# Optimization experiments

Measured on AMD Instinct MI355X. Metric: run time of the kernel, lower is better.

Reference implementation:

```python
import jax, jax.numpy as jnp
import numpy as np


def _pointnet(x, w1, b1, w2, b2, w3, b3):
    # x: [B, 3, P]; shared per-point MLP 3->64->128->128, max-pool over points -> [B,128]
    h = jax.nn.relu(jnp.einsum('oc,bcp->bop', w1, x) + b1[None, :, None])
    h = jax.nn.relu(jnp.einsum('oc,bcp->bop', w2, h) + b2[None, :, None])
    h = jax.nn.relu(jnp.einsum('oc,bcp->bop', w3, h) + b3[None, :, None])
    return h.max(axis=2)


def _lstm_layer(x, wih, whh, b):
    # x: [B, T, D]; standard LSTM (pytorch gate order i,f,g,o), returns [B, T, 128]
    B = x.shape[0]
    h0 = jnp.zeros((B, 128), x.dtype)
    def step(carry, xt):
        h, c = carry
        g = xt @ wih.T + h @ whh.T + b
        i, f, gg, o = jnp.split(g, 4, axis=-1)
        c = jax.nn.sigmoid(f) * c + jax.nn.sigmoid(i) * jnp.tanh(gg)
        h = jax.nn.sigmoid(o) * jnp.tanh(c)
        return (h, c), h
    _, hs = jax.lax.scan(step, (h0, h0), jnp.swapaxes(x, 0, 1))
    return jnp.swapaxes(hs, 0, 1)


def _edgeconv(x, aff, tw, tb, pw, pb, N):
    # DGL EdgeConv, max aggregation. Edges: det i -> track (N+j) where aff[i,j]==1, plus
    # self loops on every node. Message on edge u->v: theta(x_u - x_v) + phi(x_v).
    phi = x @ pw.T + pb                                   # [N+M, 256]
    diff = x[:N][:, None, :] - x[N:][None, :, :]          # [N, M, 256] (x_src - x_dst)
    msg = jnp.einsum('nmc,oc->nmo', diff, tw) + tb        # theta applied to diffs
    msg = jnp.where(aff[:, :, None] > 0, msg, jnp.finfo(x.dtype).min)
    h_trk = phi[N:] + jnp.maximum(tb, msg.max(axis=0))    # self-loop message is theta(0)=tb
    h_det = phi[:N] + tb                                  # dets only receive their self loop
    return jnp.concatenate([h_det, h_trk], axis=0)


def _forward(det_pc_in_box, det_boxes3d, track_pc_in_box, track_boxes3d, init_aff_matrix,
             pn_w1, pn_b1, pn_w2, pn_b2, pn_w3, pn_b3,
             mlp_w1, mlp_b1, mlp_w2, mlp_b2,
             l0_wih, l0_whh, l0_b, l1_wih, l1_whh, l1_b,
             ec_tw, ec_tb, ec_pw, ec_pb,
             er_w1, er_b1, er_w2, er_b2):
    N = det_pc_in_box.shape[0]
    det_app = _pointnet(jnp.swapaxes(det_pc_in_box, 1, 2), pn_w1, pn_b1, pn_w2, pn_b2, pn_w3, pn_b3)
    trk_app = _pointnet(jnp.swapaxes(track_pc_in_box, 1, 2), pn_w1, pn_b1, pn_w2, pn_b2, pn_w3, pn_b3)
    det_mot = jax.nn.relu(det_boxes3d @ mlp_w1.T + mlp_b1) @ mlp_w2.T + mlp_b2
    trk_mot = _lstm_layer(_lstm_layer(track_boxes3d, l0_wih, l0_whh, l0_b), l1_wih, l1_whh, l1_b)[:, -1, :]
    h = jnp.concatenate([jnp.concatenate([det_app, det_mot], axis=1),
                         jnp.concatenate([trk_app, trk_mot], axis=1)], axis=0)  # [N+M, 256]
    for k in range(4):
        h = jax.nn.relu(_edgeconv(h, init_aff_matrix, ec_tw[k], ec_tb[k], ec_pw[k], ec_pb[k], N))
    # pairwise affinity: (track - det) differences through small MLP + sigmoid (BCE head)
    edges = h[N:][None, :, :] - h[:N][:, None, :]                                # [N, M, 256]
    e = jax.nn.relu(jnp.einsum('nmc,oc->nmo', edges, er_w1) + er_b1)             # [N, M, 64]
    regr = jax.nn.sigmoid(jnp.einsum('nmo,ko->nmk', e, er_w2) + er_b2)[..., 0]   # [N, M]
    valid = init_aff_matrix * regr
    valid = jnp.where(valid == 0, jnp.asarray(99.0, valid.dtype), valid)
    return valid


def setup_inputs() -> dict:
    key = jax.random.key(0)
    ks = jax.random.split(key, 20)
    N, M, P, T = 512, 512, 256, 10
    f = jnp.float32
    def rn(k, shp):
        return jax.random.normal(k, shp, dtype=f) * 0.05
    return {
        'det_pc_in_box': jax.random.normal(ks[0], (N, P, 3), dtype=f),
        'det_boxes3d': jax.random.normal(ks[1], (N, 9), dtype=f),
        'track_pc_in_box': jax.random.normal(ks[2], (M, P, 3), dtype=f),
        'track_boxes3d': jax.random.normal(ks[3], (M, T, 9), dtype=f),
        'init_aff_matrix': jnp.ones((N, M), dtype=f),
        'gt_affinity_matrix': jnp.zeros((N, M), dtype=jnp.int32),
        'pn_w1': rn(ks[4], (64, 3)), 'pn_b1': jnp.zeros((64,), f),
        'pn_w2': rn(ks[5], (128, 64)), 'pn_b2': jnp.zeros((128,), f),
        'pn_w3': rn(ks[6], (128, 128)), 'pn_b3': jnp.zeros((128,), f),
        'mlp_w1': rn(ks[7], (64, 9)), 'mlp_b1': jnp.zeros((64,), f),
        'mlp_w2': rn(ks[8], (128, 64)), 'mlp_b2': jnp.zeros((128,), f),
        'l0_wih': rn(ks[9], (512, 9)), 'l0_whh': rn(ks[10], (512, 128)), 'l0_b': jnp.zeros((512,), f),
        'l1_wih': rn(ks[11], (512, 128)), 'l1_whh': rn(ks[12], (512, 128)), 'l1_b': jnp.zeros((512,), f),
        'ec_tw': rn(ks[13], (4, 256, 256)), 'ec_tb': jnp.zeros((4, 256), f),
        'ec_pw': rn(ks[14], (4, 256, 256)), 'ec_pb': jnp.zeros((4, 256), f),
        'er_w1': rn(ks[15], (64, 256)), 'er_b1': jnp.zeros((64,), f),
        'er_w2': rn(ks[16], (1, 64)), 'er_b2': jnp.zeros((1,), f),
    }


def reference(det_pc_in_box, det_boxes3d, track_pc_in_box, track_boxes3d, init_aff_matrix,
              gt_affinity_matrix,
              pn_w1, pn_b1, pn_w2, pn_b2, pn_w3, pn_b3,
              mlp_w1, mlp_b1, mlp_w2, mlp_b2,
              l0_wih, l0_whh, l0_b, l1_wih, l1_whh, l1_b,
              ec_tw, ec_tb, ec_pw, ec_pb,
              er_w1, er_b1, er_w2, er_b2):
    # gt_affinity_matrix is only used by the training loss; inference path ignores it.
    return _forward(det_pc_in_box, det_boxes3d, track_pc_in_box, track_boxes3d, init_aff_matrix,
                    pn_w1, pn_b1, pn_w2, pn_b2, pn_w3, pn_b3,
                    mlp_w1, mlp_b1, mlp_w2, mlp_b2,
                    l0_wih, l0_whh, l0_b, l1_wih, l1_whh, l1_b,
                    ec_tw, ec_tb, ec_pw, ec_pb,
                    er_w1, er_b1, er_w2, er_b2)
```

## Files before the change

kernel.cpp:

```cpp
#include <hip/hip_runtime.h>
#include <math.h>

#define N_DET 512
#define N_TRK 512
#define NPTS  256

typedef __attribute__((ext_vector_type(8))) short short8;
typedef __attribute__((ext_vector_type(4))) float f32x4;
typedef unsigned short ushort_t;

__device__ __forceinline__ float sigm(float x) { return 1.f / (1.f + expf(-x)); }

__device__ __forceinline__ unsigned short f2bf(float f) {
    unsigned u = __float_as_uint(f);
    u += 0x7FFF + ((u >> 16) & 1);
    return (unsigned short)(u >> 16);
}
__device__ __forceinline__ float bf2f(unsigned short h) {
    return __uint_as_float(((unsigned)h) << 16);
}

__global__ __launch_bounds__(64) void pn_wprep_kernel(
    const float* __restrict__ w2, const float* __restrict__ w3,
    unsigned short* __restrict__ wfrag)
{
    const int f = blockIdx.x;
    const int lane = threadIdx.x;
    const int lm = lane & 15, lg = lane >> 4;
    const float* src;
    if (f < 16) {
        const int s = f >> 3, n = f & 7;
        src = w2 + (size_t)(n*16 + lm)*64 + s*32 + lg*8;
    } else {
        const int f2 = f - 16, s = f2 >> 3, n = f2 & 7;
        src = w3 + (size_t)(n*16 + lm)*128 + s*32 + lg*8;
    }
    short8 v;
#pragma unroll
    for (int j = 0; j < 8; ++j) v[j] = (short)f2bf(src[j]);
    *reinterpret_cast<short8*>(wfrag + ((size_t)f*64 + lane)*8) = v;
}

__global__ __launch_bounds__(64) void ec_wprep_kernel(
    const float* __restrict__ tw, const float* __restrict__ pw,
    unsigned short* __restrict__ whi, unsigned short* __restrict__ wlo)
{
    const int id = blockIdx.x;
    const int layer = id >> 8;
    const int ntile = (id >> 3) & 31, kf = id & 7;
    const int lane = threadIdx.x;
    const int lm = lane & 15, lg = lane >> 4;
    const int col = ntile*16 + lm, k = kf*32 + lg*8;
    const float* src = (col < 256)
        ? tw + ((size_t)layer*256 + col)*256 + k
        : pw + ((size_t)layer*256 + (col - 256))*256 + k;
    short8 hi, lo;
#pragma unroll
    for (int j = 0; j < 8; ++j) {
        const float f = src[j];
        const unsigned short h = f2bf(f);
        hi[j] = (short)h;
        lo[j] = (short)f2bf(f - bf2f(h));
    }
    const size_t off = ((size_t)id*64 + lane)*8;
    *reinterpret_cast<short8*>(whi + off) = hi;
    *reinterpret_cast<short8*>(wlo + off) = lo;
}

__global__ __launch_bounds__(256) void h2bf_kernel(
    const float* __restrict__ h,
    unsigned short* __restrict__ hi, unsigned short* __restrict__ lo)
{
    const int id = blockIdx.x * 256 + threadIdx.x;
    const float4 v = *(const float4*)(h + (size_t)id*4);
    ushort_t h4[4], l4[4];
    const float vv[4] = {v.x, v.y, v.z, v.w};
#pragma unroll
    for (int j = 0; j < 4; ++j) {
        h4[j] = f2bf(vv[j]);
        l4[j] = f2bf(vv[j] - bf2f(h4[j]));
    }
    *(ulong1*)(hi + (size_t)id*4) = *(ulong1*)h4;
    *(ulong1*)(lo + (size_t)id*4) = *(ulong1*)l4;
}

__global__ __launch_bounds__(256, 1) void pointnet_mfma_kernel(
    const float* __restrict__ det_pc, const float* __restrict__ trk_pc,
    const float* __restrict__ w1, const float* __restrict__ b1,
    const unsigned short* __restrict__ wfrag,
    const float* __restrict__ b2, const float* __restrict__ b3,
    float* __restrict__ hout)
{
    __shared__ unsigned short h1s[256*72];
    __shared__ unsigned short h2s[256*136];
    __shared__ float wmaxs[4][128];

    const int tid = threadIdx.x;
    const int box = blockIdx.x;
    const int lane = tid & 63, w = tid >> 6;
    const int lm = lane & 15, lg = lane >> 4;

    const float* pc = (box < N_DET) ? det_pc + ((size_t)box*NPTS + tid)*3
                                    : trk_pc + ((size_t)(box - N_DET)*NPTS + tid)*3;
    const float x = pc[0], y = pc[1], z = pc[2];
#pragma unroll
    for (int j = 0; j < 8; ++j) {
        short8 v;
#pragma unroll
        for (int o = 0; o < 8; ++o) {
            const int ch = j*8 + o;
            float s = fmaf(w1[ch*3+0], x, fmaf(w1[ch*3+1], y,
                        fmaf(w1[ch*3+2], z, b1[ch])));
            v[o] = (short)f2bf(fmaxf(s, 0.f));
        }
        *reinterpret_cast<short8*>(&h1s[tid*72 + j*8]) = v;
    }
    __syncthreads();

    short8 w2f[16];
#pragma unroll
    for (int f = 0; f < 16; ++f)
        w2f[f] = *reinterpret_cast<const short8*>(wfrag + ((size_t)f*64 + lane)*8);
    float b2v[8];
#pragma unroll
    for (int n = 0; n < 8; ++n) b2v[n] = b2[n*16 + lm];

#pragma unroll
    for (int t = 0; t < 4; ++t) {
        const int arow = w*64 + t*16 + lm;
        const short8 a0 = *reinterpret_cast<const short8*>(&h1s[arow*72 + lg*8]);
        const short8 a1 = *reinterpret_cast<const short8*>(&h1s[arow*72 + 32 + lg*8]);
        const int wrow = w*64 + t*16 + lg*4;
#pragma unroll
        for (int n = 0; n < 8; ++n) {
            f32x4 acc = {0.f, 0.f, 0.f, 0.f};
            acc = __builtin_amdgcn_mfma_f32_16x16x32_bf16(a0, w2f[n],     acc, 0, 0, 0);
            acc = __builtin_amdgcn_mfma_f32_16x16x32_bf16(a1, w2f[8 + n], acc, 0, 0, 0);
#pragma unroll
            for (int r = 0; r < 4; ++r) {
                const float v = fmaxf(acc[r] + b2v[n], 0.f);
                h2s[(wrow + r)*136 + n*16 + lm] = f2bf(v);
            }
        }
    }
    __syncthreads();

    short8 w3f[32];
#pragma unroll
    for (int f = 0; f < 32; ++f)
        w3f[f] = *reinterpret_cast<const short8*>(wfrag + ((size_t)(16 + f)*64 + lane)*8);

    float pm[8];
#pragma unroll
    for (int n = 0; n < 8; ++n) pm[n] = -3.0e38f;

#pragma unroll
    for (int t = 0; t < 4; ++t) {
        const int arow = w*64 + t*16 + lm;
        const short8 a0 = *reinterpret_cast<const short8*>(&h2s[arow*136 +  0 + lg*8]);
        const short8 a1 = *reinterpret_cast<const short8*>(&h2s[arow*136 + 32 + lg*8]);
        const short8 a2 = *reinterpret_cast<const short8*>(&h2s[arow*136 + 64 + lg*8]);
        const short8 a3 = *reinterpret_cast<const short8*>(&h2s[arow*136 + 96 + lg*8]);
#pragma unroll
        for (int n = 0; n < 8; ++n) {
            f32x4 acc = {0.f, 0.f, 0.f, 0.f};
            acc = __builtin_amdgcn_mfma_f32_16x16x32_bf16(a0, w3f[n],      acc, 0, 0, 0);
            acc = __builtin_amdgcn_mfma_f32_16x16x32_bf16(a1, w3f[8 + n],  acc, 0, 0, 0);
            acc = __builtin_amdgcn_mfma_f32_16x16x32_bf16(a2, w3f[16 + n], acc, 0, 0, 0);
            acc = __builtin_amdgcn_mfma_f32_16x16x32_bf16(a3, w3f[24 + n], acc, 0, 0, 0);
#pragma unroll
            for (int r = 0; r < 4; ++r) pm[n] = fmaxf(pm[n], acc[r]);
        }
    }
#pragma unroll
    for (int n = 0; n < 8; ++n) {
        float v = pm[n];
        v = fmaxf(v, __shfl_xor(v, 16, 64));
        v = fmaxf(v, __shfl_xor(v, 32, 64));
        pm[n] = v;
    }
    if (lg == 0) {
#pragma unroll
        for (int n = 0; n < 8; ++n) wmaxs[w][n*16 + lm] = pm[n];
    }
    __syncthreads();
    if (tid < 128) {
        const float m = fmaxf(fmaxf(wmaxs[0][tid], wmaxs[1][tid]),
                              fmaxf(wmaxs[2][tid], wmaxs[3][tid]));
        hout[(size_t)box*256 + tid] = fmaxf(m + b3[tid], 0.f);
    }
}

__global__ __launch_bounds__(128) void detmlp_kernel(
    const float* __restrict__ boxes,
    const float* __restrict__ w1, const float* __restrict__ b1,
    const float* __restrict__ w2, const float* __restrict__ b2,
    float* __restrict__ hout)
{
    __shared__ float xb[9];
    __shared__ float h1[64];
    const int b = blockIdx.x, t = threadIdx.x;
    if (t < 9) xb[t] = boxes[b*9 + t];
    __syncthreads();
    if (t < 64) {
        float s = b1[t];
#pragma unroll
        for (int c = 0; c < 9; ++c) s = fmaf(w1[t*9+c], xb[c], s);
        h1[t] = fmaxf(s, 0.f);
    }
    __syncthreads();
    float s = b2[t];
    const float* wr = w2 + t*64;
#pragma unroll
    for (int c = 0; c < 64; ++c) s = fmaf(wr[c], h1[c], s);
    hout[(size_t)b * 256 + 128 + t] = s;
}

__global__ __launch_bounds__(256) void transpose_wih1_kernel(
    const float* __restrict__ in, float* __restrict__ out)
{
    const int id = blockIdx.x * 256 + threadIdx.x;
    const int k = id >> 9, r = id & 511;
    out[id] = in[r * 128 + k];
}

__global__ __launch_bounds__(512) void lstm_rec0_kernel(
    const float* __restrict__ xseq,
    const float* __restrict__ wih0, const float* __restrict__ whh0,
    const float* __restrict__ b0, float* __restrict__ h0seq)
{
    __shared__ float hs[128][2];
    __shared__ float xb[2][12];
    __shared__ float gs[4][2][128];
    const int r  = threadIdx.x;
    const int b2 = blockIdx.x * 2;
    const int q  = r >> 7 & 3, jj = r & 127;
    const int mb = r >> 7, mj = r & 127;

    float w[128];
#pragma unroll
    for (int k = 0; k < 128; k += 4) {
        const float4 v = *(const float4*)(whh0 + (size_t)r * 128 + k);
        w[k] = v.x; w[k+1] = v.y; w[k+2] = v.z; w[k+3] = v.w;
    }
    float wx[9];
#pragma unroll
    for (int c = 0; c < 9; ++c) wx[c] = wih0[(size_t)r * 9 + c];
    const float bias = b0[r];

    float cst = 0.f;
    if (r < 256) hs[mj][mb] = 0.f;
    __syncthreads();

    for (int t = 0; t < 10; ++t) {
        if (r < 18) xb[r / 9][r % 9] = xseq[((size_t)(b2 + r / 9) * 10 + t) * 9 + r % 9];
        __syncthreads();
        float a0 = bias, a1 = bias;
#pragma unroll
        for (int c = 0; c < 9; ++c) {
            a0 = fmaf(wx[c], xb[0][c], a0);
            a1 = fmaf(wx[c], xb[1][c], a1);
        }
#pragma unroll
        for (int k = 0; k < 128; ++k) {
            const float2 h2 = *(const float2*)&hs[k][0];
            a0 = fmaf(w[k], h2.x, a0);
            a1 = fmaf(w[k], h2.y, a1);
        }
        gs[q][0][jj] = a0;
        gs[q][1][jj] = a1;
        __syncthreads();
        if (r < 256) {
            const float gi = gs[0][mb][mj], gf = gs[1][mb][mj];
            const float gg = gs[2][mb][mj], go = gs[3][mb][mj];
            cst = sigm(gf) * cst + sigm(gi) * tanhf(gg);
            const float hn = sigm(go) * tanhf(cst);
            hs[mj][mb] = hn;
            h0seq[((size_t)(b2 + mb) * 10 + t) * 128 + mj] = hn;
        }
        __syncthreads();
    }
}

__global__ __launch_bounds__(512) void lstm_rec1_kernel(
    const float* __restrict__ h0seq, const float* __restrict__ wih1T,
    const float* __restrict__ whh1, const float* __restrict__ b1,
    float* __restrict__ hout)
{
    __shared__ float hs[128][2];
    __shared__ float xs_[128][2];
    __shared__ float gs[4][2][128];
    const int r  = threadIdx.x;
    const int b2 = blockIdx.x * 2;
    const int q  = r >> 7 & 3, jj = r & 127;
    const int mb = r >> 7, mj = r & 127;

    float w[128];
#pragma unroll
    for (int k = 0; k < 128; k += 4) {
        const float4 v = *(const float4*)(whh1 + (size_t)r * 128 + k);
        w[k] = v.x; w[k+1] = v.y; w[k+2] = v.z; w[k+3] = v.w;
    }
    const float bias = b1[r];

    float cst = 0.f;
    if (r < 256) hs[mj][mb] = 0.f;
    __syncthreads();

    for (int t = 0; t < 10; ++t) {
        if (r < 256)
            xs_[mj][mb] = h0seq[((size_t)(b2 + mb) * 10 + t) * 128 + mj];
        __syncthreads();
        float a0 = bias, a1 = bias;
#pragma unroll
        for (int k = 0; k < 128; ++k) {
            const float wxv = wih1T[k * 512 + r];
            const float2 x2 = *(const float2*)&xs_[k][0];
            const float2 h2 = *(const float2*)&hs[k][0];
            a0 = fmaf(wxv, x2.x, fmaf(w[k], h2.x, a0));
            a1 = fmaf(wxv, x2.y, fmaf(w[k], h2.y, a1));
        }
        gs[q][0][jj] = a0;
        gs[q][1][jj] = a1;
        __syncthreads();
        if (r < 256) {
            const float gi = gs[0][mb][mj], gf = gs[1][mb][mj];
            const float gg = gs[2][mb][mj], go = gs[3][mb][mj];
            cst = sigm(gf) * cst + sigm(gi) * tanhf(gg);
            const float hn = sigm(go) * tanhf(cst);
            hs[mj][mb] = hn;
            if (t == 9)
                hout[(size_t)(N_DET + b2 + mb) * 256 + 128 + mj] = hn;
        }
        __syncthreads();
    }
}

__global__ __launch_bounds__(256) void ec_gemm_mfma_kernel(
    const unsigned short* __restrict__ hhi, const unsigned short* __restrict__ hlo,
    const unsigned short* __restrict__ whi, const unsigned short* __restrict__ wlo,
    const float* __restrict__ tb, const float* __restrict__ pb,
    float* __restrict__ Abuf, float* __restrict__ Bbuf,
    float* __restrict__ phiT, float* __restrict__ hnext,
    unsigned short* __restrict__ nhi, unsigned short* __restrict__ nlo)
{
    const int bm = blockIdx.x, bn = blockIdx.y;
    const int tid = threadIdx.x, lane = tid & 63, w = tid >> 6;
    const int lm = lane & 15, lg = lane >> 4;
    const int mrow0 = bm*32 + (w & 1)*16;
    const int nt0   = bn*4 + (w >> 1)*2;
    const int arow  = mrow0 + lm;

    f32x4 acc[2] = {{0.f,0.f,0.f,0.f},{0.f,0.f,0.f,0.f}};

#pragma unroll
    for (int kf = 0; kf < 8; ++kf) {
        const short8 ahi = *reinterpret_cast<const short8*>(
            hhi + (size_t)arow*256 + kf*32 + lg*8);
        const short8 alo = *reinterpret_cast<const short8*>(
            hlo + (size_t)arow*256 + kf*32 + lg*8);
#pragma unroll
        for (int n2 = 0; n2 < 2; ++n2) {
            const size_t foff = ((size_t)((nt0 + n2)*8 + kf)*64 + lane)*8;
            const short8 bhi = *reinterpret_cast<const short8*>(whi + foff);
            const short8 blo = *reinterpret_cast<const short8*>(wlo + foff);
            acc[n2] = __builtin_amdgcn_mfma_f32_16x16x32_bf16(ahi, bhi, acc[n2], 0, 0, 0);
            acc[n2] = __builtin_amdgcn_mfma_f32_16x16x32_bf16(alo, bhi, acc[n2], 0, 0, 0);
            acc[n2] = __builtin_amdgcn_mfma_f32_16x16x32_bf16(ahi, blo, acc[n2], 0, 0, 0);
        }
    }

#pragma unroll
    for (int n2 = 0; n2 < 2; ++n2) {
        const int col = (nt0 + n2)*16 + lm;
#pragma unroll
        for (int r = 0; r < 4; ++r) {
            const int row = mrow0 + lg*4 + r;
            float v = acc[n2][r];
            if (col < 256) {
                if (row < N_DET) Abuf[(size_t)row*256 + col] = v;
                else             Bbuf[(size_t)(row - N_DET)*256 + col] = v;
            } else {
                const int o = col - 256;
                v += pb[o];
                if (row < N_DET) {
                    const float hv = fmaxf(v + tb[o], 0.f);
                    hnext[(size_t)row*256 + o] = hv;
                    const unsigned short hb = f2bf(hv);
                    nhi[(size_t)row*256 + o] = hb;
                    nlo[(size_t)row*256 + o] = f2bf(hv - bf2f(hb));
                } else {
                    phiT[(size_t)(row - N_DET)*256 + o] = v;
                }
            }
        }
    }
}

#define CM_MT 16
#define CM_OT 32
#define CM_NC 64

__global__ __launch_bounds__(256) void ec_colmax_kernel(
    const float* __restrict__ aff,
    const float* __restrict__ Abuf, const float* __restrict__ Bbuf,
    const float* __restrict__ phiT, const float* __restrict__ tb,
    float* __restrict__ hnext,
    unsigned short* __restrict__ nhi, unsigned short* __restrict__ nlo)
{
    __shared__ float As[CM_NC][CM_OT + 4];
    __shared__ float Fs[CM_NC][CM_MT + 4];
    const int t = threadIdx.x;
    const int mtile = blockIdx.x;
    const int otile = blockIdx.y;
    const int mi = t >> 4, oi = t & 15;

    float mx0 = -3.0e38f, mx1 = -3.0e38f;

    for (int n0 = 0; n0 < 512; n0 += CM_NC) {
        if (n0) __syncthreads();
        {
            const int r = t >> 3, c4 = (t & 7) * 4;
#pragma unroll
            for (int rr = 0; rr < 2; ++rr) {
                const float4 v = *(const float4*)(
                    Abuf + (size_t)(n0 + rr*32 + r)*256 + otile*CM_OT + c4);
                *(float4*)&As[rr*32 + r][c4] = v;
            }
        }
        {
            const int n = t >> 2, m4 = (t & 3) * 4;
            const float4 a = *(const float4*)(
                aff + (size_t)(n0 + n)*512 + mtile*CM_MT + m4);
            float4 f;
            f.x = (a.x > 0.f) ? 0.f : -3.0e38f;
            f.y = (a.y > 0.f) ? 0.f : -3.0e38f;
            f.z = (a.z > 0.f) ? 0.f : -3.0e38f;
            f.w = (a.w > 0.f) ? 0.f : -3.0e38f;
            *(float4*)&Fs[n][m4] = f;
        }
        __syncthreads();
#pragma unroll 4
        for (int n = 0; n < CM_NC; ++n) {
            const float f = Fs[n][mi];
            const float2 a = *(const float2*)&As[n][oi*2];
            mx0 = fmaxf(mx0, a.x + f);
            mx1 = fmaxf(mx1, a.y + f);
        }
    }

    const int m = mtile*CM_MT + mi;
    const int o = otile*CM_OT + oi*2;
    const float2 tb2 = *(const float2*)(tb + o);
    const float2 bb  = *(const float2*)(Bbuf + (size_t)m*256 + o);
    const float2 ph  = *(const float2*)(phiT + (size_t)m*256 + o);
    const float v0 = fmaxf(tb2.x, mx0 - bb.x + tb2.x);
    const float v1 = fmaxf(tb2.y, mx1 - bb.y + tb2.y);
    float2 outv;
    outv.x = fmaxf(ph.x + v0, 0.f);
    outv.y = fmaxf(ph.y + v1, 0.f);
    const size_t base = (size_t)(N_DET + m)*256 + o;
    *(float2*)(hnext + base) = outv;
    const unsigned short h0 = f2bf(outv.x), h1 = f2bf(outv.y);
    nhi[base]     = h0;
    nhi[base + 1] = h1;
    nlo[base]     = f2bf(outv.x - bf2f(h0));
    nlo[base + 1] = f2bf(outv.y - bf2f(h1));
}

__global__ __launch_bounds__(256) void headp_kernel(
    const float* __restrict__ h, const float* __restrict__ w1, float* __restrict__ P)
{
    const int tid = threadIdx.x;
    const int o = tid & 63, rl = tid >> 6;
    const int row = blockIdx.x * 4 + rl;
    const float* hr = h + (size_t)row * 256;
    const float* wr = w1 + (size_t)o * 256;
    float s0 = 0.f, s1 = 0.f, s2 = 0.f, s3 = 0.f;
#pragma unroll
    for (int c = 0; c < 256; c += 4) {
        const float4 hv = *(const float4*)(hr + c);
        const float4 wv = *(const float4*)(wr + c);
        s0 = fmaf(hv.x, wv.x, s0);
        s1 = fmaf(hv.y, wv.y, s1);
        s2 = fmaf(hv.z, wv.z, s2);
        s3 = fmaf(hv.w, wv.w, s3);
    }
    P[(size_t)row * 64 + o] = (s0 + s1) + (s2 + s3);
}

__global__ __launch_bounds__(256) void pairwise_kernel(
    const float* __restrict__ P, const float* __restrict__ aff,
    const float* __restrict__ eb1, const float* __restrict__ ew2, const float* __restrict__ eb2,
    float* __restrict__ out)
{
    __shared__ float pd[64], sb1[64], sw2[64];
    const int n = blockIdx.y;
    const int t = threadIdx.x;
    if (t < 64)       pd[t]        = P[(size_t)n * 64 + t];
    else if (t < 128) sb1[t - 64]  = eb1[t - 64];
    else if (t < 192) sw2[t - 128] = ew2[t - 128];
    __syncthreads();
    const int m = blockIdx.x * 256 + t;
    const float* pt = P + (size_t)(N_DET + m) * 64;
    float s = eb2[0];
#pragma unroll
    for (int c = 0; c < 64; c += 4) {
        const float4 pv = *(const float4*)(pt + c);
        float e;
        e = fmaxf(pv.x - pd[c+0] + sb1[c+0], 0.f); s = fmaf(e, sw2[c+0], s);
        e = fmaxf(pv.y - pd[c+1] + sb1[c+1], 0.f); s = fmaf(e, sw2[c+1], s);
        e = fmaxf(pv.z - pd[c+2] + sb1[c+2], 0.f); s = fmaf(e, sw2[c+2], s);
        e = fmaxf(pv.w - pd[c+3] + sb1[c+3], 0.f); s = fmaf(e, sw2[c+3], s);
    }
    const float r = 1.f / (1.f + expf(-s));
    const float v = aff[(size_t)n * 512 + m] * r;
    out[(size_t)n * 512 + m] = (v == 0.f) ? 99.f : v;
}

extern "C" void kernel_launch(void* const* d_in, const int* in_sizes, int n_in,
                              void* d_out, int out_size, void* d_ws, size_t ws_size,
                              hipStream_t stream)
{
    (void)in_sizes; (void)n_in; (void)out_size; (void)ws_size;

    const float* det_pc  = (const float*)d_in[0];
    const float* det_box = (const float*)d_in[1];
    const float* trk_pc  = (const float*)d_in[2];
    const float* trk_box = (const float*)d_in[3];
    const float* aff     = (const float*)d_in[4];
    const float* pn_w1  = (const float*)d_in[6];
    const float* pn_b1  = (const float*)d_in[7];
    const float* pn_w2  = (const float*)d_in[8];
    const float* pn_b2  = (const float*)d_in[9];
    const float* pn_w3  = (const float*)d_in[10];
    const float* pn_b3  = (const float*)d_in[11];
    const float* mlp_w1 = (const float*)d_in[12];
    const float* mlp_b1 = (const float*)d_in[13];
    const float* mlp_w2 = (const float*)d_in[14];
    const float* mlp_b2 = (const float*)d_in[15];
    const float* l0_wih = (const float*)d_in[16];
    const float* l0_whh = (const float*)d_in[17];
    const float* l0_b   = (const float*)d_in[18];
    const float* l1_wih = (const float*)d_in[19];
    const float* l1_whh = (const float*)d_in[20];
    const float* l1_b   = (const float*)d_in[21];
    const float* ec_tw  = (const float*)d_in[22];
    const float* ec_tb  = (const float*)d_in[23];
    const float* ec_pw  = (const float*)d_in[24];
    const float* ec_pb  = (const float*)d_in[25];
    const float* er_w1  = (const float*)d_in[26];
    const float* er_b1  = (const float*)d_in[27];
    const float* er_w2  = (const float*)d_in[28];
    const float* er_b2  = (const float*)d_in[29];

    float* ws    = (float*)d_ws;
    float* hA    = ws;
    float* hB    = hA + 1024*256;
    float* Abuf  = hB + 1024*256;
    float* Bbuf  = Abuf + 512*256;
    float* phiT  = Bbuf + 512*256;
    float* P     = phiT + 512*256;
    float* h0seq = P + 1024*64;
    float* wih1T = h0seq + 512*10*128;
    unsigned short* wfrag = (unsigned short*)(wih1T + 128*512);
    unsigned short* ecwhi = wfrag + 48*64*8;
    unsigned short* ecwlo = ecwhi + 1024*64*8;
    unsigned short* hbfA_hi = ecwlo + 1024*64*8;
    unsigned short* hbfA_lo = hbfA_hi + 1024*256;
    unsigned short* hbfB_hi = hbfA_lo + 1024*256;
    unsigned short* hbfB_lo = hbfB_hi + 1024*256;

    pn_wprep_kernel<<<48, 64, 0, stream>>>(pn_w2, pn_w3, wfrag);
    ec_wprep_kernel<<<1024, 64, 0, stream>>>(ec_tw, ec_pw, ecwhi, ecwlo);
    pointnet_mfma_kernel<<<1024, 256, 0, stream>>>(det_pc, trk_pc, pn_w1, pn_b1,
                                                   wfrag, pn_b2, pn_b3, hA);
    detmlp_kernel<<<512, 128, 0, stream>>>(det_box, mlp_w1, mlp_b1, mlp_w2, mlp_b2, hA);
    transpose_wih1_kernel<<<256, 256, 0, stream>>>(l1_wih, wih1T);
    lstm_rec0_kernel<<<256, 512, 0, stream>>>(trk_box, l0_wih, l0_whh, l0_b, h0seq);
    lstm_rec1_kernel<<<256, 512, 0, stream>>>(h0seq, wih1T, l1_whh, l1_b, hA);
    h2bf_kernel<<<256, 256, 0, stream>>>(hA, hbfA_hi, hbfA_lo);

    float* hcur = hA;  float* hnext = hB;
    unsigned short* chi = hbfA_hi; unsigned short* clo = hbfA_lo;
    unsigned short* nhi = hbfB_hi; unsigned short* nlo = hbfB_lo;
    for (int k = 0; k < 4; ++k) {
        const float* tb = ec_tb + (size_t)k * 256;
        const float* pb = ec_pb + (size_t)k * 256;
        ec_gemm_mfma_kernel<<<dim3(32, 8), 256, 0, stream>>>(
            chi, clo, ecwhi + (size_t)k*256*64*8, ecwlo + (size_t)k*256*64*8,
            tb, pb, Abuf, Bbuf, phiT, hnext, nhi, nlo);
        ec_colmax_kernel<<<dim3(32, 8), 256, 0, stream>>>(aff, Abuf, Bbuf, phiT, tb,
                                                          hnext, nhi, nlo);
        float* tf = hcur; hcur = hnext; hnext = tf;
        unsigned short* th = chi; chi = nhi; nhi = th;
        unsigned short* tl = clo; clo = nlo; nlo = tl;
    }

    headp_kernel<<<256, 256, 0, stream>>>(hcur, er_w1, P);
    pairwise_kernel<<<dim3(2, 512), 256, 0, stream>>>(P, aff, er_b1, er_w2, er_b2,
                                                      (float*)d_out);
}
```

Measured before the change: 382.5 us.

## Rewrite LSTM layers with MFMA recurrence and hoisted input projections

Replaces the scalar-FMA LSTM recurrence kernels with a bf16 MFMA version. Each block handles 16 sequences, keeps the hidden state as hi/lo bf16 fragments in shared memory, and stores recurrent weights pre-swizzled into bf16 fragments. The input-to-gate projections for both layers are computed up front for all timesteps, using a small FMA kernel for layer 0 and an MFMA GEMM for layer 1, so the serial loop only does the hidden-state matmul. The aim is to cut the long serial recurrence cost and move the input GEMMs out of the time loop. In exchange the recurrent weights are rounded to a single bf16 value (only activations get hi/lo splitting), which reduces precision, and only 32 blocks run the recurrence.

```diff
diff --git a/kernel.cpp b/kernel.cpp
--- a/kernel.cpp
+++ b/kernel.cpp
@@ -67,6 +67,164 @@
     *reinterpret_cast<short8*>(wlo + off) = lo;
 }
 
+__global__ __launch_bounds__(64) void lstm_wprep_kernel(
+    const float* __restrict__ whh0, const float* __restrict__ wih1,
+    const float* __restrict__ whh1, unsigned short* __restrict__ wf)
+{
+    const int id = blockIdx.x;
+    const int mat = id >> 7, rest = id & 127;
+    const int nt = rest >> 2, kf = rest & 3;
+    const int lane = threadIdx.x;
+    const int lm = lane & 15, lg = lane >> 4;
+    const float* src = (mat == 0) ? whh0 : ((mat == 1) ? wih1 : whh1);
+    const float* p = src + (size_t)(nt*16 + lm)*128 + kf*32 + lg*8;
+    short8 v;
+#pragma unroll
+    for (int j = 0; j < 8; ++j) v[j] = (short)f2bf(p[j]);
+    *reinterpret_cast<short8*>(wf + ((size_t)id*64 + lane)*8) = v;
+}
+
+__global__ __launch_bounds__(512) void lstm_xg0_kernel(
+    const float* __restrict__ xseq, const float* __restrict__ wih0,
+    float* __restrict__ xg0)
+{
+    __shared__ float xs[8][12];
+    const int tid = threadIdx.x;
+    const int m0 = blockIdx.x * 8;
+    if (tid < 72) xs[tid / 9][tid % 9] = xseq[(size_t)m0*9 + tid];
+    float wx[9];
+#pragma unroll
+    for (int c = 0; c < 9; ++c) wx[c] = wih0[tid*9 + c];
+    __syncthreads();
+#pragma unroll
+    for (int i = 0; i < 8; ++i) {
+        float s = 0.f;
+#pragma unroll
+        for (int c = 0; c < 9; ++c) s = fmaf(wx[c], xs[i][c], s);
+        xg0[(size_t)(m0 + i)*512 + tid] = s;
+    }
+}
+
+__global__ __launch_bounds__(256) void lstm_xg1_kernel(
+    const unsigned short* __restrict__ h0hi, const unsigned short* __restrict__ h0lo,
+    const unsigned short* __restrict__ wfrag, float* __restrict__ xg1)
+{
+    const int tid = threadIdx.x, lane = tid & 63, w = tid >> 6;
+    const int lm = lane & 15, lg = lane >> 4;
+    const int m0 = blockIdx.x*64 + w*16;
+    const int bn = blockIdx.y;
+    const int arow = m0 + lm;
+    short8 ahi[4], alo[4];
+#pragma unroll
+    for (int kf = 0; kf < 4; ++kf) {
+        ahi[kf] = *reinterpret_cast<const short8*>(h0hi + (size_t)arow*128 + kf*32 + lg*8);
+        alo[kf] = *reinterpret_cast<const short8*>(h0lo + (size_t)arow*128 + kf*32 + lg*8);
+    }
+#pragma unroll
+    for (int nt = 0; nt < 4; ++nt) {
+        f32x4 acc = {0.f, 0.f, 0.f, 0.f};
+#pragma unroll
+        for (int kf = 0; kf < 4; ++kf) {
+            const short8 bf = *reinterpret_cast<const short8*>(
+                wfrag + ((size_t)((bn*4 + nt)*4 + kf)*64 + lane)*8);
+            acc = __builtin_amdgcn_mfma_f32_16x16x32_bf16(ahi[kf], bf, acc, 0, 0, 0);
+            acc = __builtin_amdgcn_mfma_f32_16x16x32_bf16(alo[kf], bf, acc, 0, 0, 0);
+        }
+#pragma unroll
+        for (int r = 0; r < 4; ++r)
+            xg1[(size_t)(m0 + lg*4 + r)*512 + bn*64 + nt*16 + lm] = acc[r];
+    }
+}
+
+template<int LAYER>
+__global__ __launch_bounds__(512, 2) void lstm_mfma_kernel(
+    const unsigned short* __restrict__ wfrag,
+    const float* __restrict__ xg, const float* __restrict__ bias,
+    unsigned short* __restrict__ h0hi, unsigned short* __restrict__ h0lo,
+    float* __restrict__ hout)
+{
+    __shared__ unsigned short hfhi[4*64*8];
+    __shared__ unsigned short hflo[4*64*8];
+    __shared__ float gs[512*20];
+
+    const int tid = threadIdx.x;
+    const int lane = tid & 63, w = tid >> 6;
+    const int lm = lane & 15, lg = lane >> 4;
+    const int b0 = blockIdx.x * 16;
+
+    short8 wf[4][4];
+#pragma unroll
+    for (int nt = 0; nt < 4; ++nt)
+#pragma unroll
+        for (int kf = 0; kf < 4; ++kf)
+            wf[nt][kf] = *reinterpret_cast<const short8*>(
+                wfrag + ((size_t)((w*4 + nt)*4 + kf)*64 + lane)*8);
+
+    for (int i = tid; i < 2048; i += 512) { hfhi[i] = 0; hflo[i] = 0; }
+
+    const int mj = tid & 127;
+    const int mb0 = (tid >> 7) * 4;
+    const float bi = bias[mj], bf_ = bias[128 + mj];
+    const float bg = bias[256 + mj], bo = bias[384 + mj];
+    const int hkf = mj >> 5, hlg = (mj >> 3) & 3, hjj = mj & 7;
+    float c[4] = {0.f, 0.f, 0.f, 0.f};
+
+    __syncthreads();
+
+    for (int t = 0; t < 10; ++t) {
+        float xgv[4][4];
+#pragma unroll
+        for (int s = 0; s < 4; ++s) {
+            const size_t btg = ((size_t)(b0 + mb0 + s)*10 + t)*512;
+            xgv[s][0] = xg[btg + mj];
+            xgv[s][1] = xg[btg + 128 + mj];
+            xgv[s][2] = xg[btg + 256 + mj];
+            xgv[s][3] = xg[btg + 384 + mj];
+        }
+        short8 ahi[4], alo[4];
+#pragma unroll
+        for (int kf = 0; kf < 4; ++kf) {
+            ahi[kf] = *reinterpret_cast<const short8*>(&hfhi[(kf*64 + lane)*8]);
+            alo[kf] = *reinterpret_cast<const short8*>(&hflo[(kf*64 + lane)*8]);
+        }
+#pragma unroll
+        for (int nt = 0; nt < 4; ++nt) {
+            f32x4 acc = {0.f, 0.f, 0.f, 0.f};
+#pragma unroll
+            for (int kf = 0; kf < 4; ++kf) {
+                acc = __builtin_amdgcn_mfma_f32_16x16x32_bf16(ahi[kf], wf[nt][kf], acc, 0, 0, 0);
+                acc = __builtin_amdgcn_mfma_f32_16x16x32_bf16(alo[kf], wf[nt][kf], acc, 0, 0, 0);
+            }
+            const int g = w*64 + nt*16 + lm;
+            float4 tmp; tmp.x = acc[0]; tmp.y = acc[1]; tmp.z = acc[2]; tmp.w = acc[3];
+            *(float4*)&gs[g*20 + lg*4] = tmp;
+        }
+        __syncthreads();
+#pragma unroll
+        for (int s = 0; s < 4; ++s) {
+            const int b = mb0 + s;
+            const float gi = gs[mj*20 + b]         + xgv[s][0] + bi;
+            const float gf = gs[(128 + mj)*20 + b] + xgv[s][1] + bf_;
+            const float gg = gs[(256 + mj)*20 + b] + xgv[s][2] + bg;
+            const float go = gs[(384 + mj)*20 + b] + xgv[s][3] + bo;
+            c[s] = sigm(gf)*c[s] + sigm(gi)*tanhf(gg);
+            const float hn = sigm(go)*tanhf(c[s]);
+            const unsigned short hh = f2bf(hn);
+            const unsigned short hl = f2bf(hn - bf2f(hh));
+            hfhi[(hkf*64 + hlg*16 + b)*8 + hjj] = hh;
+            hflo[(hkf*64 + hlg*16 + b)*8 + hjj] = hl;
+            if constexpr (LAYER == 0) {
+                h0hi[((size_t)(b0 + b)*10 + t)*128 + mj] = hh;
+                h0lo[((size_t)(b0 + b)*10 + t)*128 + mj] = hl;
+            } else {
+                if (t == 9)
+                    hout[(size_t)(N_DET + b0 + b)*256 + 128 + mj] = hn;
+            }
+        }
+        __syncthreads();
+    }
+}
+
 __global__ __launch_bounds__(256) void h2bf_kernel(
     const float* __restrict__ h,
     unsigned short* __restrict__ hi, unsigned short* __restrict__ lo)
@@ -214,126 +372,6 @@
 #pragma unroll
     for (int c = 0; c < 64; ++c) s = fmaf(wr[c], h1[c], s);
     hout[(size_t)b * 256 + 128 + t] = s;
-}
-
-__global__ __launch_bounds__(256) void transpose_wih1_kernel(
-    const float* __restrict__ in, float* __restrict__ out)
-{
-    const int id = blockIdx.x * 256 + threadIdx.x;
-    const int k = id >> 9, r = id & 511;
-    out[id] = in[r * 128 + k];
-}
-
-__global__ __launch_bounds__(512) void lstm_rec0_kernel(
-    const float* __restrict__ xseq,
-    const float* __restrict__ wih0, const float* __restrict__ whh0,
-    const float* __restrict__ b0, float* __restrict__ h0seq)
-{
-    __shared__ float hs[128][2];
-    __shared__ float xb[2][12];
-    __shared__ float gs[4][2][128];
-    const int r  = threadIdx.x;
-    const int b2 = blockIdx.x * 2;
-    const int q  = r >> 7 & 3, jj = r & 127;
-    const int mb = r >> 7, mj = r & 127;
-
-    float w[128];
-#pragma unroll
-    for (int k = 0; k < 128; k += 4) {
-        const float4 v = *(const float4*)(whh0 + (size_t)r * 128 + k);
-        w[k] = v.x; w[k+1] = v.y; w[k+2] = v.z; w[k+3] = v.w;
-    }
-    float wx[9];
-#pragma unroll
-    for (int c = 0; c < 9; ++c) wx[c] = wih0[(size_t)r * 9 + c];
-    const float bias = b0[r];
-
-    float cst = 0.f;
-    if (r < 256) hs[mj][mb] = 0.f;
-    __syncthreads();
-
-    for (int t = 0; t < 10; ++t) {
-        if (r < 18) xb[r / 9][r % 9] = xseq[((size_t)(b2 + r / 9) * 10 + t) * 9 + r % 9];
-        __syncthreads();
-        float a0 = bias, a1 = bias;
-#pragma unroll
-        for (int c = 0; c < 9; ++c) {
-            a0 = fmaf(wx[c], xb[0][c], a0);
-            a1 = fmaf(wx[c], xb[1][c], a1);
-        }
-#pragma unroll
-        for (int k = 0; k < 128; ++k) {
-            const float2 h2 = *(const float2*)&hs[k][0];
-            a0 = fmaf(w[k], h2.x, a0);
-            a1 = fmaf(w[k], h2.y, a1);
-        }
-        gs[q][0][jj] = a0;
-        gs[q][1][jj] = a1;
-        __syncthreads();
-        if (r < 256) {
-            const float gi = gs[0][mb][mj], gf = gs[1][mb][mj];
-            const float gg = gs[2][mb][mj], go = gs[3][mb][mj];
-            cst = sigm(gf) * cst + sigm(gi) * tanhf(gg);
-            const float hn = sigm(go) * tanhf(cst);
-            hs[mj][mb] = hn;
-            h0seq[((size_t)(b2 + mb) * 10 + t) * 128 + mj] = hn;
-        }
-        __syncthreads();
-    }
-}
-
-__global__ __launch_bounds__(512) void lstm_rec1_kernel(
-    const float* __restrict__ h0seq, const float* __restrict__ wih1T,
-    const float* __restrict__ whh1, const float* __restrict__ b1,
-    float* __restrict__ hout)
-{
-    __shared__ float hs[128][2];
-    __shared__ float xs_[128][2];
-    __shared__ float gs[4][2][128];
-    const int r  = threadIdx.x;
-    const int b2 = blockIdx.x * 2;
-    const int q  = r >> 7 & 3, jj = r & 127;
-    const int mb = r >> 7, mj = r & 127;
-
-    float w[128];
-#pragma unroll
-    for (int k = 0; k < 128; k += 4) {
-        const float4 v = *(const float4*)(whh1 + (size_t)r * 128 + k);
-        w[k] = v.x; w[k+1] = v.y; w[k+2] = v.z; w[k+3] = v.w;
-    }
-    const float bias = b1[r];
-
-    float cst = 0.f;
-    if (r < 256) hs[mj][mb] = 0.f;
-    __syncthreads();
-
-    for (int t = 0; t < 10; ++t) {
-        if (r < 256)
-            xs_[mj][mb] = h0seq[((size_t)(b2 + mb) * 10 + t) * 128 + mj];
-        __syncthreads();
-        float a0 = bias, a1 = bias;
-#pragma unroll
-        for (int k = 0; k < 128; ++k) {
-            const float wxv = wih1T[k * 512 + r];
-            const float2 x2 = *(const float2*)&xs_[k][0];
-            const float2 h2 = *(const float2*)&hs[k][0];
-            a0 = fmaf(wxv, x2.x, fmaf(w[k], h2.x, a0));
-            a1 = fmaf(wxv, x2.y, fmaf(w[k], h2.y, a1));
-        }
-        gs[q][0][jj] = a0;
-        gs[q][1][jj] = a1;
-        __syncthreads();
-        if (r < 256) {
-            const float gi = gs[0][mb][mj], gf = gs[1][mb][mj];
-            const float gg = gs[2][mb][mj], go = gs[3][mb][mj];
-            cst = sigm(gf) * cst + sigm(gi) * tanhf(gg);
-            const float hn = sigm(go) * tanhf(cst);
-            hs[mj][mb] = hn;
-            if (t == 9)
-                hout[(size_t)(N_DET + b2 + mb) * 256 + 128 + mj] = hn;
-        }
-        __syncthreads();
-    }
 }
 
 __global__ __launch_bounds__(256) void ec_gemm_mfma_kernel(
@@ -561,24 +599,32 @@
     float* Bbuf  = Abuf + 512*256;
     float* phiT  = Bbuf + 512*256;
     float* P     = phiT + 512*256;
-    float* h0seq = P + 1024*64;
-    float* wih1T = h0seq + 512*10*128;
-    unsigned short* wfrag = (unsigned short*)(wih1T + 128*512);
-    unsigned short* ecwhi = wfrag + 48*64*8;
-    unsigned short* ecwlo = ecwhi + 1024*64*8;
-    unsigned short* hbfA_hi = ecwlo + 1024*64*8;
+    float* xg0   = P + 1024*64;
+    float* xg1   = xg0 + 5120*512;
+    unsigned short* wfrag  = (unsigned short*)(xg1 + 5120*512);
+    unsigned short* ecwhi  = wfrag + 48*64*8;
+    unsigned short* ecwlo  = ecwhi + 1024*64*8;
+    unsigned short* lstmwf = ecwlo + 1024*64*8;
+    unsigned short* h0hi   = lstmwf + 3*128*64*8;
+    unsigned short* h0lo   = h0hi + 5120*128;
+    unsigned short* hbfA_hi = h0lo + 5120*128;
     unsigned short* hbfA_lo = hbfA_hi + 1024*256;
     unsigned short* hbfB_hi = hbfA_lo + 1024*256;
     unsigned short* hbfB_lo = hbfB_hi + 1024*256;
 
     pn_wprep_kernel<<<48, 64, 0, stream>>>(pn_w2, pn_w3, wfrag);
     ec_wprep_kernel<<<1024, 64, 0, stream>>>(ec_tw, ec_pw, ecwhi, ecwlo);
+    lstm_wprep_kernel<<<384, 64, 0, stream>>>(l0_whh, l1_wih, l1_whh, lstmwf);
     pointnet_mfma_kernel<<<1024, 256, 0, stream>>>(det_pc, trk_pc, pn_w1, pn_b1,
                                                    wfrag, pn_b2, pn_b3, hA);
     detmlp_kernel<<<512, 128, 0, stream>>>(det_box, mlp_w1, mlp_b1, mlp_w2, mlp_b2, hA);
-    transpose_wih1_kernel<<<256, 256, 0, stream>>>(l1_wih, wih1T);
-    lstm_rec0_kernel<<<256, 512, 0, stream>>>(trk_box, l0_wih, l0_whh, l0_b, h0seq);
-    lstm_rec1_kernel<<<256, 512, 0, stream>>>(h0seq, wih1T, l1_whh, l1_b, hA);
+
+    lstm_xg0_kernel<<<640, 512, 0, stream>>>(trk_box, l0_wih, xg0);
+    lstm_mfma_kernel<0><<<32, 512, 0, stream>>>(lstmwf, xg0, l0_b, h0hi, h0lo, nullptr);
+    lstm_xg1_kernel<<<dim3(80, 8), 256, 0, stream>>>(h0hi, h0lo, lstmwf + 128*64*8, xg1);
+    lstm_mfma_kernel<1><<<32, 512, 0, stream>>>(lstmwf + 2*128*64*8, xg1, l1_b,
+                                                nullptr, nullptr, hA);
+
     h2bf_kernel<<<256, 256, 0, stream>>>(hA, hbfA_hi, hbfA_lo);
 
     float* hcur = hA;  float* hnext = hB;
```

Result: faster. 349.3 us (-8.7%).
